# Performance work log

Measured on AMD Instinct MI355X. Metric: run time of the kernel, lower is better.

Reference implementation:

```python
import jax, jax.numpy as jnp
import numpy as np

E = 1024   # embed_dim
H = 16     # num_heads
HD = E // H
FF = 4096  # hidden_dim
EPS = 1e-5

def _ln(x, g, b):
    mu = jnp.mean(x, axis=-1, keepdims=True)
    var = jnp.mean((x - mu) ** 2, axis=-1, keepdims=True)
    return (x - mu) * jax.lax.rsqrt(var + EPS) * g + b

def setup_inputs() -> dict:
    key = jax.random.key(0)
    ks = jax.random.split(key, 8)
    s = 0.02
    return {
        "x": jax.random.normal(ks[0], (2, 2048, E), dtype=jnp.float32),
        "w_qkv": jax.random.normal(ks[1], (3 * E, E), dtype=jnp.float32) * s,
        "b_qkv": jnp.zeros((3 * E,), dtype=jnp.float32),
        "w_out": jax.random.normal(ks[2], (E, E), dtype=jnp.float32) * s,
        "b_out": jnp.zeros((E,), dtype=jnp.float32),
        "g1": jnp.ones((E,), dtype=jnp.float32),
        "beta1": jnp.zeros((E,), dtype=jnp.float32),
        "g2": jnp.ones((E,), dtype=jnp.float32),
        "beta2": jnp.zeros((E,), dtype=jnp.float32),
        "w1": jax.random.normal(ks[3], (FF, E), dtype=jnp.float32) * s,
        "bf1": jnp.zeros((FF,), dtype=jnp.float32),
        "w2": jax.random.normal(ks[4], (E, FF), dtype=jnp.float32) * s,
        "bf2": jnp.zeros((E,), dtype=jnp.float32),
    }

def reference(x, w_qkv, b_qkv, w_out, b_out, g1, beta1, g2, beta2, w1, bf1, w2, bf2):
    B, S, _ = x.shape
    # qkv projection, then the module's exact reshape: (B,S,H,3*HD) -> (H,B,S,3*HD)
    qkv = (x @ w_qkv.T + b_qkv).reshape(B, S, H, 3 * HD).transpose(2, 0, 1, 3)
    q, k, v = jnp.split(qkv, 3, axis=-1)           # each (H,B,S,HD)
    scores = jnp.einsum('hbqd,hbkd->hbqk', q, k) / (HD ** 0.5)
    attn = jax.nn.softmax(scores, axis=-1)
    ctx = jnp.einsum('hbqk,hbkd->hbqd', attn, v)   # (H,B,S,HD)
    ctx = ctx.transpose(1, 2, 0, 3).reshape(B, S, E)
    attn_out = ctx @ w_out.T + b_out
    x1 = _ln(x + attn_out, g1, beta1)
    # FFN with exact (erf-based) GELU, matching torch nn.GELU default
    h = jax.nn.gelu(x1 @ w1.T + bf1, approximate=False)
    ffn_out = h @ w2.T + bf2
    return _ln(x1 + ffn_out, g2, beta2)
```

## Files before the change

kernel.cpp:

```cpp
#include <hip/hip_runtime.h>
#include <hip/hip_bf16.h>
#include <math.h>

typedef __bf16 bf16x8 __attribute__((ext_vector_type(8)));
typedef __bf16 bf16x4 __attribute__((ext_vector_type(4)));
typedef float  f32x4  __attribute__((ext_vector_type(4)));

#define MFMA16(a, b, c) __builtin_amdgcn_mfma_f32_16x16x32_bf16((a), (b), (c), 0, 0, 0)

__device__ __forceinline__ void gl16(const void* g, void* l) {
  __builtin_amdgcn_global_load_lds(
      (const __attribute__((address_space(1))) unsigned int*)g,
      (__attribute__((address_space(3))) unsigned int*)l, 16, 0, 0);
}

__global__ __launch_bounds__(256) void cast_all(
    const float* __restrict__ x, const float* __restrict__ wqkv,
    const float* __restrict__ wout, const float* __restrict__ w1,
    const float* __restrict__ w2, __bf16* __restrict__ xb,
    __bf16* __restrict__ wqkvb, __bf16* __restrict__ woutb,
    __bf16* __restrict__ w1b, __bf16* __restrict__ w2b) {
  const long i = ((long)blockIdx.x * 256 + threadIdx.x) * 4;
  const float* src;
  __bf16* dst;
  long off;
  if (i < 4194304L) { src = x; dst = xb; off = i; }
  else if (i < 7340032L) { src = wqkv; dst = wqkvb; off = i - 4194304L; }
  else if (i < 8388608L) { src = wout; dst = woutb; off = i - 7340032L; }
  else if (i < 12582912L) { src = w1; dst = w1b; off = i - 8388608L; }
  else { src = w2; dst = w2b; off = i - 12582912L; }
  const float4 f = *(const float4*)(src + off);
  bf16x4 o = {(__bf16)f.x, (__bf16)f.y, (__bf16)f.z, (__bf16)f.w};
  *(bf16x4*)(dst + off) = o;
}

template <int MODE>
__global__ __launch_bounds__(256, 2) void gemm_bt(
    const __bf16* __restrict__ A, const __bf16* __restrict__ Bw,
    const float* __restrict__ bias, __bf16* __restrict__ outB,
    int M, int N, int K) {
  __shared__ __bf16 As[128 * 32];
  __shared__ __bf16 Bs[128 * 32];
  const int tid = threadIdx.x;
  const int wave = tid >> 6, lane = tid & 63;
  const int quad = lane >> 4, l16 = lane & 15;
  const int wm = (wave >> 1) * 64, wn = (wave & 1) * 64;
  const long bm = (long)blockIdx.y * 128, bn = (long)blockIdx.x * 128;
  const int r0 = tid >> 2;
  const int c0 = (tid & 3) * 8;
  const __bf16* Ag = A + (bm + r0) * (long)K + c0;
  const __bf16* Bg = Bw + (bn + r0) * (long)K + c0;

  f32x4 acc[4][4] = {};

  for (int k0 = 0; k0 < K; k0 += 32) {
    __syncthreads();
    gl16(Ag + k0, &As[tid * 8]);
    gl16(Ag + 64 * (long)K + k0, &As[2048 + tid * 8]);
    gl16(Bg + k0, &Bs[tid * 8]);
    gl16(Bg + 64 * (long)K + k0, &Bs[2048 + tid * 8]);
    __syncthreads();

    bf16x8 af[4], bfr[4];
#pragma unroll
    for (int mt = 0; mt < 4; mt++)
      af[mt] = *(const bf16x8*)&As[(wm + mt * 16 + l16) * 32 + quad * 8];
#pragma unroll
    for (int nt = 0; nt < 4; nt++)
      bfr[nt] = *(const bf16x8*)&Bs[(wn + nt * 16 + l16) * 32 + quad * 8];
#pragma unroll
    for (int nt = 0; nt < 4; nt++)
#pragma unroll
      for (int mt = 0; mt < 4; mt++)
        acc[mt][nt] = MFMA16(af[mt], bfr[nt], acc[mt][nt]);
  }

#pragma unroll
  for (int mt = 0; mt < 4; mt++) {
#pragma unroll
    for (int nt = 0; nt < 4; nt++) {
#pragma unroll
      for (int r = 0; r < 4; r++) {
        const int row = (int)bm + wm + mt * 16 + quad * 4 + r;
        const int col = (int)bn + wn + nt * 16 + l16;
        float v = acc[mt][nt][r] + bias[col];
        if (MODE == 0) {
          const int b = row >> 11, s = row & 2047;
          const int h = col / 192, rem = col - h * 192;
          const int seg = rem >> 6, d = rem & 63;
          const int hb = h * 2 + b;
          if (seg == 0) {
            v *= 0.180336880111113704f;
            outB[((long)hb * 2048 + s) * 64 + d] = (__bf16)v;
          } else if (seg == 1) {
            outB[4194304L + ((long)hb * 2048 + s) * 64 + d] = (__bf16)v;
          } else {
            const int t = s >> 6, kp = s & 63;
            outB[2 * 4194304L + (((long)hb * 32 + t) * 64 + d) * 64 + kp] = (__bf16)v;
          }
        } else {
          const float g = 0.5f * v * (1.0f + erff(v * 0.70710678118654752f));
          outB[(long)row * N + col] = (__bf16)g;
        }
      }
    }
  }
}

__global__ __launch_bounds__(256, 2) void gemm_split(
    const __bf16* __restrict__ A, const __bf16* __restrict__ Bw,
    __bf16* __restrict__ Pbase, const long4 offs, int N, int K, int splitK) {
  __shared__ __bf16 As[128 * 32];
  __shared__ __bf16 Bs[128 * 32];
  const int tid = threadIdx.x;
  const int wave = tid >> 6, lane = tid & 63;
  const int quad = lane >> 4, l16 = lane & 15;
  const int wm = (wave >> 1) * 64, wn = (wave & 1) * 64;
  const long bm = (long)blockIdx.y * 128, bn = (long)blockIdx.x * 128;
  const int z = blockIdx.z;
  const long kb = (long)z * splitK;
  const int r0 = tid >> 2;
  const int c0 = (tid & 3) * 8;
  const __bf16* Ag = A + (bm + r0) * (long)K + c0 + kb;
  const __bf16* Bg = Bw + (bn + r0) * (long)K + c0 + kb;

  f32x4 acc[4][4] = {};

  for (int k0 = 0; k0 < splitK; k0 += 32) {
    __syncthreads();
    gl16(Ag + k0, &As[tid * 8]);
    gl16(Ag + 64 * (long)K + k0, &As[2048 + tid * 8]);
    gl16(Bg + k0, &Bs[tid * 8]);
    gl16(Bg + 64 * (long)K + k0, &Bs[2048 + tid * 8]);
    __syncthreads();

    bf16x8 af[4], bfr[4];
#pragma unroll
    for (int mt = 0; mt < 4; mt++)
      af[mt] = *(const bf16x8*)&As[(wm + mt * 16 + l16) * 32 + quad * 8];
#pragma unroll
    for (int nt = 0; nt < 4; nt++)
      bfr[nt] = *(const bf16x8*)&Bs[(wn + nt * 16 + l16) * 32 + quad * 8];
#pragma unroll
    for (int nt = 0; nt < 4; nt++)
#pragma unroll
      for (int mt = 0; mt < 4; mt++)
        acc[mt][nt] = MFMA16(af[mt], bfr[nt], acc[mt][nt]);
  }

  const long po = (z == 0) ? offs.x : (z == 1) ? offs.y : (z == 2) ? offs.z : offs.w;
#pragma unroll
  for (int mt = 0; mt < 4; mt++)
#pragma unroll
    for (int nt = 0; nt < 4; nt++)
#pragma unroll
      for (int r = 0; r < 4; r++) {
        const int row = (int)bm + wm + mt * 16 + quad * 4 + r;
        const int col = (int)bn + wn + nt * 16 + l16;
        Pbase[po + (long)row * N + col] = (__bf16)acc[mt][nt][r];
      }
}

template <int WB>
__global__ __launch_bounds__(256) void reduce_ln(
    const __bf16* __restrict__ Pbase, const long4 offs,
    const float* __restrict__ resid, const float* __restrict__ bias,
    const float* __restrict__ g, const float* __restrict__ be,
    float* __restrict__ outF, __bf16* __restrict__ outB) {
  const int tid = threadIdx.x;
  const long row = blockIdx.x;
  const int c = tid * 4;
  float4 v = ((const float4*)(resid + row * 1024))[tid];
  const float4 bb = ((const float4*)bias)[tid];
  v.x += bb.x; v.y += bb.y; v.z += bb.z; v.w += bb.w;
  const long lo[4] = {offs.x, offs.y, offs.z, offs.w};
#pragma unroll
  for (int s = 0; s < 4; s++) {
    const bf16x4 p = *(const bf16x4*)&Pbase[lo[s] + row * 1024 + c];
    v.x += (float)p[0]; v.y += (float)p[1]; v.z += (float)p[2]; v.w += (float)p[3];
  }
  float sum = v.x + v.y + v.z + v.w;
  float sq = v.x * v.x + v.y * v.y + v.z * v.z + v.w * v.w;
#pragma unroll
  for (int m = 32; m >= 1; m >>= 1) {
    sum += __shfl_xor(sum, m);
    sq += __shfl_xor(sq, m);
  }
  __shared__ float red[8];
  const int wave = tid >> 6;
  if ((tid & 63) == 0) {
    red[wave] = sum;
    red[4 + wave] = sq;
  }
  __syncthreads();
  sum = red[0] + red[1] + red[2] + red[3];
  sq = red[4] + red[5] + red[6] + red[7];
  const float mu = sum * (1.f / 1024.f);
  const float var = sq * (1.f / 1024.f) - mu * mu;
  const float rs = rsqrtf(var + 1e-5f);
  const float4 gv = ((const float4*)g)[tid];
  const float4 bv = ((const float4*)be)[tid];
  float4 o;
  o.x = (v.x - mu) * rs * gv.x + bv.x;
  o.y = (v.y - mu) * rs * gv.y + bv.y;
  o.z = (v.z - mu) * rs * gv.z + bv.z;
  o.w = (v.w - mu) * rs * gv.w + bv.w;
  ((float4*)(outF + row * 1024))[tid] = o;
  if (WB) {
    bf16x4 ob = {(__bf16)o.x, (__bf16)o.y, (__bf16)o.z, (__bf16)o.w};
    *(bf16x4*)&outB[row * 1024 + c] = ob;
  }
}

__global__ __launch_bounds__(256) void flash_attn(const __bf16* __restrict__ Qb,
                                                  const __bf16* __restrict__ Kb,
                                                  const __bf16* __restrict__ Vtb,
                                                  __bf16* __restrict__ ctx) {
  __shared__ __bf16 KsLo[64 * 32], KsHi[64 * 32];
  __shared__ __bf16 VsLo[64 * 32], VsHi[64 * 32];
  __shared__ __bf16 Pb[4][32 * 72];
  const int tid = threadIdx.x;
  const int wave = tid >> 6, lane = tid & 63;
  const int quad = lane >> 4, l16 = lane & 15;
  const int n = blockIdx.x;
  const int hb = n & 31;
  const int qblk = n >> 5;
  const int h = hb >> 1, b = hb & 1;
  const __bf16* Q = Qb + (long)hb * 131072;
  const __bf16* K = Kb + (long)hb * 131072;
  const __bf16* Vt = Vtb + (long)hb * 131072;
  const int qr = qblk * 128 + wave * 32;

  bf16x8 q0[2], q1[2];
#pragma unroll
  for (int rb = 0; rb < 2; rb++) {
    q0[rb] = *(const bf16x8*)&Q[(qr + rb * 16 + l16) * 64 + quad * 8];
    q1[rb] = *(const bf16x8*)&Q[(qr + rb * 16 + l16) * 64 + 32 + quad * 8];
  }

  f32x4 o[2][4] = {};
  f32x4 lp[2] = {};

  const int sr = tid >> 2;
  const int sc = (tid & 3) * 8;

  for (int kt = 0; kt < 2048; kt += 64) {
    __syncthreads();
    gl16(&K[(kt + sr) * 64 + sc], &KsLo[tid * 8]);
    gl16(&K[(kt + sr) * 64 + 32 + sc], &KsHi[tid * 8]);
    const __bf16* Vtile = Vt + (long)(kt >> 6) * 4096;
    gl16(&Vtile[sr * 64 + sc], &VsLo[tid * 8]);
    gl16(&Vtile[sr * 64 + 32 + sc], &VsHi[tid * 8]);
    __syncthreads();

    bf16x8 kf0[4], kf1[4];
#pragma unroll
    for (int nt = 0; nt < 4; nt++) {
      kf0[nt] = *(const bf16x8*)&KsLo[(nt * 16 + l16) * 32 + quad * 8];
      kf1[nt] = *(const bf16x8*)&KsHi[(nt * 16 + l16) * 32 + quad * 8];
    }
    f32x4 s[2][4];
#pragma unroll
    for (int rb = 0; rb < 2; rb++)
#pragma unroll
      for (int nt = 0; nt < 4; nt++) {
        f32x4 z = {};
        z = MFMA16(q0[rb], kf0[nt], z);
        z = MFMA16(q1[rb], kf1[nt], z);
        s[rb][nt] = z;
      }

#pragma unroll
    for (int rb = 0; rb < 2; rb++)
#pragma unroll
      for (int nt = 0; nt < 4; nt++)
#pragma unroll
        for (int r = 0; r < 4; r++) {
          const float p = __builtin_amdgcn_exp2f(s[rb][nt][r]);
          s[rb][nt][r] = p;
          lp[rb][r] += p;
        }

#pragma unroll
    for (int rb = 0; rb < 2; rb++)
#pragma unroll
      for (int nt = 0; nt < 4; nt++)
#pragma unroll
        for (int r = 0; r < 4; r++)
          Pb[wave][(rb * 16 + quad * 4 + r) * 72 + nt * 16 + l16] =
              (__bf16)s[rb][nt][r];

    bf16x8 vf0[4], vf1[4];
#pragma unroll
    for (int nt = 0; nt < 4; nt++) {
      vf0[nt] = *(const bf16x8*)&VsLo[(nt * 16 + l16) * 32 + quad * 8];
      vf1[nt] = *(const bf16x8*)&VsHi[(nt * 16 + l16) * 32 + quad * 8];
    }
#pragma unroll
    for (int rb = 0; rb < 2; rb++) {
      const bf16x8 p0 = *(const bf16x8*)&Pb[wave][(rb * 16 + l16) * 72 + quad * 8];
      const bf16x8 p1 = *(const bf16x8*)&Pb[wave][(rb * 16 + l16) * 72 + 32 + quad * 8];
#pragma unroll
      for (int nt = 0; nt < 4; nt++) {
        o[rb][nt] = MFMA16(p0, vf0[nt], o[rb][nt]);
        o[rb][nt] = MFMA16(p1, vf1[nt], o[rb][nt]);
      }
    }
  }

#pragma unroll
  for (int rb = 0; rb < 2; rb++) {
    float inv[4];
#pragma unroll
    for (int r = 0; r < 4; r++) {
      float l = lp[rb][r];
      l += __shfl_xor(l, 1);
      l += __shfl_xor(l, 2);
      l += __shfl_xor(l, 4);
      l += __shfl_xor(l, 8);
      inv[r] = __builtin_amdgcn_rcpf(l);
    }
#pragma unroll
    for (int nt = 0; nt < 4; nt++)
#pragma unroll
      for (int r = 0; r < 4; r++) {
        const int srow = qr + rb * 16 + quad * 4 + r;
        const float val = o[rb][nt][r] * inv[r];
        const int d = nt * 16 + l16;
        ctx[((long)(b * 2048 + srow)) * 1024 + h * 64 + d] = (__bf16)val;
      }
  }
}

extern "C" void kernel_launch(void* const* d_in, const int* in_sizes, int n_in,
                              void* d_out, int out_size, void* d_ws, size_t ws_size,
                              hipStream_t stream) {
  const float* x     = (const float*)d_in[0];
  const float* w_qkv = (const float*)d_in[1];
  const float* b_qkv = (const float*)d_in[2];
  const float* w_out = (const float*)d_in[3];
  const float* b_out = (const float*)d_in[4];
  const float* g1    = (const float*)d_in[5];
  const float* be1   = (const float*)d_in[6];
  const float* g2    = (const float*)d_in[7];
  const float* be2   = (const float*)d_in[8];
  const float* w1    = (const float*)d_in[9];
  const float* bf1   = (const float*)d_in[10];
  const float* w2    = (const float*)d_in[11];
  const float* bf2   = (const float*)d_in[12];
  float* out = (float*)d_out;

  char* ws = (char*)d_ws;
  const long MB = 1024L * 1024;
  __bf16* wsb   = (__bf16*)ws;
  __bf16* wqkvb = (__bf16*)(ws + 0 * MB);
  __bf16* woutb = (__bf16*)(ws + 6 * MB);
  __bf16* w1b   = (__bf16*)(ws + 8 * MB);
  __bf16* w2b   = (__bf16*)(ws + 16 * MB);
  __bf16* xb    = (__bf16*)(ws + 24 * MB);
  __bf16* qkvb  = (__bf16*)(ws + 32 * MB);
  __bf16* ctxb  = (__bf16*)(ws + 56 * MB);
  float*  res1  = (float*)(ws + 64 * MB);
  __bf16* x1b   = (__bf16*)(ws + 80 * MB);
  __bf16* hb    = (__bf16*)(ws + 24 * MB);

  const long4 offs_op = {24 * 524288L, 32 * 524288L, 40 * 524288L, 48 * 524288L};
  const long4 offs_f2 = {0 * 524288L, 8 * 524288L, 56 * 524288L, 80 * 524288L};

  cast_all<<<16384, 256, 0, stream>>>(x, w_qkv, w_out, w1, w2,
                                      xb, wqkvb, woutb, w1b, w2b);

  gemm_bt<0><<<dim3(24, 32), 256, 0, stream>>>(xb, wqkvb, b_qkv, qkvb,
                                               4096, 3072, 1024);
  flash_attn<<<512, 256, 0, stream>>>(qkvb, qkvb + 4194304,
                                      qkvb + 2 * 4194304, ctxb);
  gemm_split<<<dim3(8, 32, 4), 256, 0, stream>>>(ctxb, woutb, wsb, offs_op,
                                                 1024, 1024, 256);
  reduce_ln<1><<<4096, 256, 0, stream>>>(wsb, offs_op, x, b_out, g1, be1,
                                         res1, x1b);
  gemm_bt<2><<<dim3(32, 32), 256, 0, stream>>>(x1b, w1b, bf1, hb,
                                               4096, 4096, 1024);
  gemm_split<<<dim3(8, 32, 4), 256, 0, stream>>>(hb, w2b, wsb, offs_f2,
                                                 1024, 4096, 1024);
  reduce_ln<0><<<4096, 256, 0, stream>>>(wsb, offs_f2, res1, bf2, g2, be2,
                                         out, nullptr);
}
```

Before: 369.5 us.

## Enlarge GEMM tiles to 256x256 with 8 waves and repad attention P buffer

New measurement: 404.7 us. +9.5%, slower.

```diff
diff --git a/kernel.cpp b/kernel.cpp
--- a/kernel.cpp
+++ b/kernel.cpp
@@ -35,35 +35,35 @@
 }
 
 template <int MODE>
-__global__ __launch_bounds__(256, 2) void gemm_bt(
+__global__ __launch_bounds__(512, 2) void gemm256(
     const __bf16* __restrict__ A, const __bf16* __restrict__ Bw,
     const float* __restrict__ bias, __bf16* __restrict__ outB,
     int M, int N, int K) {
-  __shared__ __bf16 As[128 * 32];
-  __shared__ __bf16 Bs[128 * 32];
+  __shared__ __bf16 As[256 * 32];
+  __shared__ __bf16 Bs[256 * 32];
   const int tid = threadIdx.x;
   const int wave = tid >> 6, lane = tid & 63;
   const int quad = lane >> 4, l16 = lane & 15;
-  const int wm = (wave >> 1) * 64, wn = (wave & 1) * 64;
-  const long bm = (long)blockIdx.y * 128, bn = (long)blockIdx.x * 128;
+  const int wm = (wave >> 2) * 128, wn = (wave & 3) * 64;
+  const long bm = (long)blockIdx.y * 256, bn = (long)blockIdx.x * 256;
   const int r0 = tid >> 2;
   const int c0 = (tid & 3) * 8;
   const __bf16* Ag = A + (bm + r0) * (long)K + c0;
   const __bf16* Bg = Bw + (bn + r0) * (long)K + c0;
 
-  f32x4 acc[4][4] = {};
+  f32x4 acc[8][4] = {};
 
   for (int k0 = 0; k0 < K; k0 += 32) {
     __syncthreads();
     gl16(Ag + k0, &As[tid * 8]);
-    gl16(Ag + 64 * (long)K + k0, &As[2048 + tid * 8]);
+    gl16(Ag + 128 * (long)K + k0, &As[4096 + tid * 8]);
     gl16(Bg + k0, &Bs[tid * 8]);
-    gl16(Bg + 64 * (long)K + k0, &Bs[2048 + tid * 8]);
-    __syncthreads();
-
-    bf16x8 af[4], bfr[4];
-#pragma unroll
-    for (int mt = 0; mt < 4; mt++)
+    gl16(Bg + 128 * (long)K + k0, &Bs[4096 + tid * 8]);
+    __syncthreads();
+
+    bf16x8 af[8], bfr[4];
+#pragma unroll
+    for (int mt = 0; mt < 8; mt++)
       af[mt] = *(const bf16x8*)&As[(wm + mt * 16 + l16) * 32 + quad * 8];
 #pragma unroll
     for (int nt = 0; nt < 4; nt++)
@@ -71,12 +71,12 @@
 #pragma unroll
     for (int nt = 0; nt < 4; nt++)
 #pragma unroll
-      for (int mt = 0; mt < 4; mt++)
+      for (int mt = 0; mt < 8; mt++)
         acc[mt][nt] = MFMA16(af[mt], bfr[nt], acc[mt][nt]);
   }
 
 #pragma unroll
-  for (int mt = 0; mt < 4; mt++) {
+  for (int mt = 0; mt < 8; mt++) {
 #pragma unroll
     for (int nt = 0; nt < 4; nt++) {
 #pragma unroll
@@ -107,6 +107,60 @@
   }
 }
 
+__global__ __launch_bounds__(512, 2) void gemm256_split(
+    const __bf16* __restrict__ A, const __bf16* __restrict__ Bw,
+    __bf16* __restrict__ Pbase, const long4 offs, int N, int K, int splitK) {
+  __shared__ __bf16 As[256 * 32];
+  __shared__ __bf16 Bs[256 * 32];
+  const int tid = threadIdx.x;
+  const int wave = tid >> 6, lane = tid & 63;
+  const int quad = lane >> 4, l16 = lane & 15;
+  const int wm = (wave >> 2) * 128, wn = (wave & 3) * 64;
+  const long bm = (long)blockIdx.y * 256, bn = (long)blockIdx.x * 256;
+  const int z = blockIdx.z;
+  const long kb = (long)z * splitK;
+  const int r0 = tid >> 2;
+  const int c0 = (tid & 3) * 8;
+  const __bf16* Ag = A + (bm + r0) * (long)K + c0 + kb;
+  const __bf16* Bg = Bw + (bn + r0) * (long)K + c0 + kb;
+
+  f32x4 acc[8][4] = {};
+
+  for (int k0 = 0; k0 < splitK; k0 += 32) {
+    __syncthreads();
+    gl16(Ag + k0, &As[tid * 8]);
+    gl16(Ag + 128 * (long)K + k0, &As[4096 + tid * 8]);
+    gl16(Bg + k0, &Bs[tid * 8]);
+    gl16(Bg + 128 * (long)K + k0, &Bs[4096 + tid * 8]);
+    __syncthreads();
+
+    bf16x8 af[8], bfr[4];
+#pragma unroll
+    for (int mt = 0; mt < 8; mt++)
+      af[mt] = *(const bf16x8*)&As[(wm + mt * 16 + l16) * 32 + quad * 8];
+#pragma unroll
+    for (int nt = 0; nt < 4; nt++)
+      bfr[nt] = *(const bf16x8*)&Bs[(wn + nt * 16 + l16) * 32 + quad * 8];
+#pragma unroll
+    for (int nt = 0; nt < 4; nt++)
+#pragma unroll
+      for (int mt = 0; mt < 8; mt++)
+        acc[mt][nt] = MFMA16(af[mt], bfr[nt], acc[mt][nt]);
+  }
+
+  const long po = (z == 0) ? offs.x : (z == 1) ? offs.y : (z == 2) ? offs.z : offs.w;
+#pragma unroll
+  for (int mt = 0; mt < 8; mt++)
+#pragma unroll
+    for (int nt = 0; nt < 4; nt++)
+#pragma unroll
+      for (int r = 0; r < 4; r++) {
+        const int row = (int)bm + wm + mt * 16 + quad * 4 + r;
+        const int col = (int)bn + wn + nt * 16 + l16;
+        Pbase[po + (long)row * N + col] = (__bf16)acc[mt][nt][r];
+      }
+}
+
 __global__ __launch_bounds__(256, 2) void gemm_split(
     const __bf16* __restrict__ A, const __bf16* __restrict__ Bw,
     __bf16* __restrict__ Pbase, const long4 offs, int N, int K, int splitK) {
@@ -218,7 +272,7 @@
                                                   __bf16* __restrict__ ctx) {
   __shared__ __bf16 KsLo[64 * 32], KsHi[64 * 32];
   __shared__ __bf16 VsLo[64 * 32], VsHi[64 * 32];
-  __shared__ __bf16 Pb[4][32 * 72];
+  __shared__ __bf16 Pb[4][32 * 68];
   const int tid = threadIdx.x;
   const int wave = tid >> 6, lane = tid & 63;
   const int quad = lane >> 4, l16 = lane & 15;
@@ -287,7 +341,7 @@
       for (int nt = 0; nt < 4; nt++)
 #pragma unroll
         for (int r = 0; r < 4; r++)
-          Pb[wave][(rb * 16 + quad * 4 + r) * 72 + nt * 16 + l16] =
+          Pb[wave][(rb * 16 + quad * 4 + r) * 68 + nt * 16 + l16] =
               (__bf16)s[rb][nt][r];
 
     bf16x8 vf0[4], vf1[4];
@@ -298,8 +352,13 @@
     }
 #pragma unroll
     for (int rb = 0; rb < 2; rb++) {
-      const bf16x8 p0 = *(const bf16x8*)&Pb[wave][(rb * 16 + l16) * 72 + quad * 8];
-      const bf16x8 p1 = *(const bf16x8*)&Pb[wave][(rb * 16 + l16) * 72 + 32 + quad * 8];
+      const int pbase = (rb * 16 + l16) * 68;
+      const bf16x4 pa0 = *(const bf16x4*)&Pb[wave][pbase + quad * 8];
+      const bf16x4 pa1 = *(const bf16x4*)&Pb[wave][pbase + quad * 8 + 4];
+      const bf16x4 pb0 = *(const bf16x4*)&Pb[wave][pbase + 32 + quad * 8];
+      const bf16x4 pb1 = *(const bf16x4*)&Pb[wave][pbase + 32 + quad * 8 + 4];
+      const bf16x8 p0 = __builtin_shufflevector(pa0, pa1, 0, 1, 2, 3, 4, 5, 6, 7);
+      const bf16x8 p1 = __builtin_shufflevector(pb0, pb1, 0, 1, 2, 3, 4, 5, 6, 7);
 #pragma unroll
       for (int nt = 0; nt < 4; nt++) {
         o[rb][nt] = MFMA16(p0, vf0[nt], o[rb][nt]);
@@ -370,7 +429,7 @@
   cast_all<<<16384, 256, 0, stream>>>(x, w_qkv, w_out, w1, w2,
                                       xb, wqkvb, woutb, w1b, w2b);
 
-  gemm_bt<0><<<dim3(24, 32), 256, 0, stream>>>(xb, wqkvb, b_qkv, qkvb,
+  gemm256<0><<<dim3(12, 16), 512, 0, stream>>>(xb, wqkvb, b_qkv, qkvb,
                                                4096, 3072, 1024);
   flash_attn<<<512, 256, 0, stream>>>(qkvb, qkvb + 4194304,
                                       qkvb + 2 * 4194304, ctxb);
@@ -378,10 +437,10 @@
                                                  1024, 1024, 256);
   reduce_ln<1><<<4096, 256, 0, stream>>>(wsb, offs_op, x, b_out, g1, be1,
                                          res1, x1b);
-  gemm_bt<2><<<dim3(32, 32), 256, 0, stream>>>(x1b, w1b, bf1, hb,
+  gemm256<2><<<dim3(16, 16), 512, 0, stream>>>(x1b, w1b, bf1, hb,
                                                4096, 4096, 1024);
-  gemm_split<<<dim3(8, 32, 4), 256, 0, stream>>>(hb, w2b, wsb, offs_f2,
-                                                 1024, 4096, 1024);
+  gemm256_split<<<dim3(4, 16, 4), 512, 0, stream>>>(hb, w2b, wsb, offs_f2,
+                                                    1024, 4096, 1024);
   reduce_ln<0><<<4096, 256, 0, stream>>>(wsb, offs_f2, res1, bf2, g2, be2,
                                          out, nullptr);
 }
```
